# Kernel tuning notes

Hardware: AMD Instinct MI355X
Metric: run time of the kernel (lower is better)

## Reference

```python
import jax, jax.numpy as jnp
import numpy as np

N = 40000      # nodes
E = 320000     # edges (no self loops in input; layer adds them)
F_IN = 256
H1, C1 = 4, 128   # layer 1: att_type 'gat', concat=True
H2, C2 = 8, 6     # layer 2: att_type 'linear', concat=False (mean over heads)
BN_EPS = 1e-5
NEG_SLOPE = 0.2


def setup_inputs() -> dict:
    key = jax.random.key(0)
    k = jax.random.split(key, 12)
    x = jax.random.normal(k[0], (N, F_IN), dtype=jnp.float32)
    row = jax.random.randint(k[1], (E,), 0, N)
    off = jax.random.randint(k[2], (E,), 1, N)
    col = (row + off) % N  # guarantees no self-loops (remove_self_loops is then a no-op)
    edge_index = jnp.stack([row, col])
    s1 = 1.0 / np.sqrt(F_IN)
    s2 = 1.0 / np.sqrt(H1 * C1)
    return dict(
        x=x,
        edge_index=edge_index,
        bn1_gamma=jnp.ones((F_IN,), jnp.float32),
        bn1_beta=jnp.zeros((F_IN,), jnp.float32),
        bn1_mean=jax.random.normal(k[3], (F_IN,), jnp.float32) * 0.1,
        bn1_var=jax.random.uniform(k[4], (F_IN,), jnp.float32, 0.5, 1.5),
        W1=jax.random.normal(k[5], (F_IN, H1 * C1), jnp.float32) * s1,
        att1=jax.random.normal(k[6], (1, H1, 2 * C1), jnp.float32) * 0.1,
        b1=jnp.zeros((H1 * C1,), jnp.float32),
        bn2_gamma=jnp.ones((H1 * C1,), jnp.float32),
        bn2_beta=jnp.zeros((H1 * C1,), jnp.float32),
        bn2_mean=jax.random.normal(k[7], (H1 * C1,), jnp.float32) * 0.1,
        bn2_var=jax.random.uniform(k[8], (H1 * C1,), jnp.float32, 0.5, 1.5),
        W2=jax.random.normal(k[9], (H1 * C1, H2 * C2), jnp.float32) * s2,
        att2=jax.random.normal(k[10], (1, H2, 2 * C2), jnp.float32) * 0.1,
        b2=jnp.zeros((C2,), jnp.float32),
    )


def _bn_eval(x, gamma, beta, mean, var):
    # BatchNorm1d in eval mode (running statistics)
    return (x - mean) * (gamma / jnp.sqrt(var + BN_EPS)) + beta


def _segment_softmax(alpha, seg, num_segments):
    # stable softmax over edges grouped by destination node
    m = jax.ops.segment_max(alpha, seg, num_segments=num_segments)
    ex = jnp.exp(alpha - m[seg])
    den = jax.ops.segment_sum(ex, seg, num_segments=num_segments)
    return ex / (den[seg] + 1e-16)


def _geo_layer(x, row, col, W, att, bias, heads, out_c, att_type, concat):
    n = x.shape[0]
    h = (x @ W).reshape(n, heads, out_c)  # [N,H,C]
    h_j = h[col]                          # gather source features per edge [E,H,C]
    if att_type == 'gat':
        # (cat([x_i,x_j]) * att).sum(-1) == per-node left/right projections gathered
        a_i = (h * att[:, :, :out_c]).sum(-1)[row]   # [E,H]
        a_j = (h_j * att[:, :, out_c:]).sum(-1)      # [E,H]
        alpha = jax.nn.leaky_relu(a_i + a_j, NEG_SLOPE)
    elif att_type == 'linear':
        al = (h_j * att[:, :, :out_c]).sum(-1)
        ar = (h_j * att[:, :, out_c:]).sum(-1)
        alpha = jnp.tanh(al + ar)
    else:
        raise ValueError(att_type)
    alpha = _segment_softmax(alpha, row, n)          # neighbor softmax
    msg = h_j * alpha[:, :, None]                    # [E,H,C]
    out = jax.ops.segment_sum(msg, row, num_segments=n)  # scatter-add ('sum' agg)
    if concat:
        out = out.reshape(n, heads * out_c)
    else:
        out = out.mean(axis=1)
    return out + bias


def reference(x, edge_index, bn1_gamma, bn1_beta, bn1_mean, bn1_var, W1, att1, b1,
              bn2_gamma, bn2_beta, bn2_mean, bn2_var, W2, att2, b2):
    n = x.shape[0]
    loop = jnp.arange(n, dtype=edge_index.dtype)
    row = jnp.concatenate([edge_index[0], loop])  # add self loops (input has none)
    col = jnp.concatenate([edge_index[1], loop])
    # layer 1: dropout (identity in eval) -> BN -> GeoLayer(gat) -> act 'linear' (identity)
    out = _bn_eval(x, bn1_gamma, bn1_beta, bn1_mean, bn1_var)
    out = _geo_layer(out, row, col, W1, att1, b1, H1, C1, 'gat', True)
    # layer 2: BN -> GeoLayer(linear) -> elu
    out = _bn_eval(out, bn2_gamma, bn2_beta, bn2_mean, bn2_var)
    out = jax.nn.elu(_geo_layer(out, row, col, W2, att2, b2, H2, C2, 'linear', False))
    return jax.nn.log_softmax(out, axis=1)
```

## Files before the change

### kernel.cpp

```cpp
#include <hip/hip_runtime.h>
#include <math.h>

#define NN   40000
#define NP   40064
#define EE   320000
#define ET   (EE + NN)
#define FIN  256
#define D1   512
#define NEG  0.2f
#define CAP  64

typedef unsigned short ushort;
typedef __attribute__((ext_vector_type(8))) short   s16x8;
typedef __attribute__((ext_vector_type(4))) float   f32x4;
typedef __attribute__((ext_vector_type(4))) unsigned short u16x4;

#define GL16(g,s) __builtin_amdgcn_global_load_lds((const __attribute__((address_space(1))) unsigned*)(g), (__attribute__((address_space(3))) unsigned*)(s), 16, 0, 0)

__device__ __forceinline__ float lrelu(float x){ return x > 0.f ? x : NEG*x; }
__device__ __forceinline__ float b2f(ushort u){ return __uint_as_float(((unsigned)u) << 16); }
__device__ __forceinline__ ushort f2bf(float f){
  unsigned u = __float_as_uint(f);
  return (ushort)((u + 0x7fffu + ((u >> 16) & 1u)) >> 16);
}
__device__ __forceinline__ float wmaxf(float v){
#pragma unroll
  for (int o = 32; o > 0; o >>= 1) v = fmaxf(v, __shfl_xor(v, o));
  return v;
}
__device__ __forceinline__ float wsumf(float v){
#pragma unroll
  for (int o = 32; o > 0; o >>= 1) v += __shfl_xor(v, o);
  return v;
}

__global__ __launch_bounds__(1024) void zero_prep_kernel(int* __restrict__ cnt,
                            const float* __restrict__ g1, const float* __restrict__ be1,
                            const float* __restrict__ mu1, const float* __restrict__ va1,
                            const float* __restrict__ g2, const float* __restrict__ be2,
                            const float* __restrict__ mu2, const float* __restrict__ va2,
                            const float* __restrict__ b1,
                            float* __restrict__ sc1, float* __restrict__ sh1,
                            float* __restrict__ sc2, float* __restrict__ sh2)
{
  int i = blockIdx.x*1024 + threadIdx.x;
  if (i < NN) cnt[i] = 0;
  if (blockIdx.x == 0){
    int t = threadIdx.x;
    if (t < FIN){ float s = g1[t]*rsqrtf(va1[t]+1e-5f); sc1[t]=s; sh1[t]=be1[t]-mu1[t]*s; }
    if (t < D1){ float s = g2[t]*rsqrtf(va2[t]+1e-5f); sc2[t]=s; sh2[t]=be2[t]+(b1[t]-mu2[t])*s; }
  }
}

__global__ __launch_bounds__(256) void prep_all_kernel(
    const int* __restrict__ rows, const int* __restrict__ cols,
    int* __restrict__ cnt, int* __restrict__ cs,
    const float* __restrict__ W1, const float* __restrict__ W2,
    const float* __restrict__ sc1, const float* __restrict__ sh1,
    const float* __restrict__ sc2, const float* __restrict__ sh2,
    const float* __restrict__ att1, const float* __restrict__ att2,
    ushort* __restrict__ K1T, float* __restrict__ k0v,
    float* __restrict__ c2, float* __restrict__ a2s)
{
  int b = blockIdx.x;
  if (b < 1407){
    int e = b*256 + threadIdx.x;
    if (e >= ET) return;
    int r, c;
    if (e < EE){ r = rows[e]; c = cols[e]; } else { r = e - EE; c = r; }
    int slot = atomicAdd(&cnt[r], 1);
    if (slot < CAP) cs[(r << 6) + slot] = c;
    return;
  }
  if (b < 1631){
    __shared__ float wcol[128];
    __shared__ float red[4];
    int t = b - 1407;
    int k = threadIdx.x;
    float val = 0.f;
    if (t < 200){
      int h;
      if (t < 192){
        h = t & 3; int j = t >> 2;
        if (k < 128){ int kk = h*128 + k; wcol[k] = W2[(size_t)kk*48 + j] * sc2[kk]; }
      } else {
        h = (t - 192) & 3; int off = ((t - 192) >= 4) ? 128 : 0;
        if (k < 128) wcol[k] = att1[h*256 + off + k];
      }
      __syncthreads();
      const float* wr = W1 + (size_t)k*D1 + h*128;
#pragma unroll
      for (int kk = 0; kk < 128; kk += 4){
        float4 wv = *(const float4*)(wr + kk);
        float4 cv = *(const float4*)(wcol + kk);
        val += wv.x*cv.x + wv.y*cv.y + wv.z*cv.z + wv.w*cv.w;
      }
      K1T[(size_t)t*FIN + k] = f2bf(val * sc1[k]);
      float part = wsumf(sh1[k] * val);
      if ((k & 63) == 0) red[k >> 6] = part;
      __syncthreads();
      if (k == 0) k0v[t] = red[0] + red[1] + red[2] + red[3];
    } else {
      K1T[(size_t)t*FIN + k] = 0;
      if (k == 0) k0v[t] = 0.f;
    }
    return;
  }
  {
    int bb = b - 1631;
    if (bb == 0 && threadIdx.x < 48){
      int h = threadIdx.x/6, c = threadIdx.x%6;
      a2s[threadIdx.x] = att2[h*12 + c] + att2[h*12 + 6 + c];
    }
    int w = bb*4 + (threadIdx.x >> 6);
    int lane = threadIdx.x & 63;
    if (w >= 48) return;
    float acc = 0.f;
    for (int k = lane; k < D1; k += 64) acc += sh2[k] * W2[(size_t)k*48 + w];
    acc = wsumf(acc);
    if (lane == 0) c2[w] = acc;
  }
}

__global__ __launch_bounds__(256) void gemmG_mfma(const float* __restrict__ X,
                                                  const ushort* __restrict__ K1T,
                                                  const float* __restrict__ k0v,
                                                  ushort* __restrict__ G,
                                                  float* __restrict__ ai,
                                                  float* __restrict__ aj)
{
  __shared__ ushort As[128*64];
  __shared__ ushort Bs[224*64];
  int row0 = blockIdx.x * 128;
  int tid = threadIdx.x, lane = tid & 63, wave = tid >> 6;
  f32x4 acc[2][13] = {};
  int srow = lane >> 3;
  int scolb = (lane & 7) * 16;
#pragma unroll
  for (int kt = 0; kt < 4; ++kt){
    int k0 = kt*64;
#pragma unroll
    for (int j = 0; j < 4; ++j){
      int c = wave*4 + j;
      int rl = c*8 + srow;
      int rowg = row0 + rl; if (rowg >= NN) rowg = 0;
      int j0 = ((lane & 7) ^ (rl & 7)) * 8;
      const float* src = X + (size_t)rowg*FIN + k0 + j0;
      float4 v0 = *(const float4*)src;
      float4 v1 = *(const float4*)(src + 4);
      s16x8 o;
      o[0]=(short)f2bf(v0.x); o[1]=(short)f2bf(v0.y); o[2]=(short)f2bf(v0.z); o[3]=(short)f2bf(v0.w);
      o[4]=(short)f2bf(v1.x); o[5]=(short)f2bf(v1.y); o[6]=(short)f2bf(v1.z); o[7]=(short)f2bf(v1.w);
      *(s16x8*)((char*)As + c*1024 + lane*16) = o;
    }
#pragma unroll
    for (int j = 0; j < 7; ++j){
      int c = wave*7 + j;
      int row = c*8 + srow;
      int cb = scolb ^ ((row & 7) << 4);
      GL16((const char*)(K1T + (size_t)row*FIN + k0) + cb, (char*)Bs + c*1024);
    }
    __syncthreads();
#pragma unroll
    for (int kk = 0; kk < 2; ++kk){
      int kb = kk*64 + (lane >> 4)*16;
      s16x8 a[2];
#pragma unroll
      for (int mi = 0; mi < 2; ++mi){
        int row = wave*32 + mi*16 + (lane & 15);
        a[mi] = *(const s16x8*)((const char*)As + row*128 + (kb ^ ((row & 7) << 4)));
      }
#pragma unroll
      for (int ni = 0; ni < 13; ++ni){
        int row = ni*16 + (lane & 15);
        s16x8 bfrag = *(const s16x8*)((const char*)Bs + row*128 + (kb ^ ((row & 7) << 4)));
#pragma unroll
        for (int mi = 0; mi < 2; ++mi)
          acc[mi][ni] = __builtin_amdgcn_mfma_f32_16x16x32_bf16(a[mi], bfrag, acc[mi][ni], 0, 0, 0);
      }
    }
    __syncthreads();
  }
  int cl = lane & 15;
#pragma unroll
  for (int mi = 0; mi < 2; ++mi){
#pragma unroll
    for (int ni = 0; ni < 12; ++ni){
      int t = ni*16 + cl;
      float kc = k0v[t];
#pragma unroll
      for (int rr = 0; rr < 4; ++rr){
        int row = row0 + wave*32 + mi*16 + (lane >> 4)*4 + rr;
        G[(size_t)row*192 + t] = f2bf(acc[mi][ni][rr] + kc);
      }
    }
    if (cl < 8){
      float kc = k0v[192 + cl];
#pragma unroll
      for (int rr = 0; rr < 4; ++rr){
        int row = row0 + wave*32 + mi*16 + (lane >> 4)*4 + rr;
        float v = acc[mi][12][rr] + kc;
        if (cl < 4) ai[(size_t)row*4 + cl] = v;
        else        aj[(size_t)row*4 + (cl-4)] = v;
      }
    }
  }
}

__global__ __launch_bounds__(256) void aggA_kernel(const ushort* __restrict__ G,
                                                   const float* __restrict__ ai,
                                                   const float* __restrict__ aj,
                                                   const int* __restrict__ cnt,
                                                   const int* __restrict__ cs,
                                                   const float* __restrict__ c2,
                                                   const float* __restrict__ a2s,
                                                   ushort* __restrict__ PE)
{
  __shared__ float wsh[4][64][4];
  __shared__ int   csh[4][64];
  int lane = threadIdx.x & 63;
  int wave = threadIdx.x >> 6;
  int n = blockIdx.x*4 + wave;
  int deg = cnt[n]; deg = deg > CAP ? CAP : deg;
  float4 an = *(const float4*)(ai + (size_t)n*4);
  bool aclane = lane < 48;
  int lidx = aclane ? lane : 0;
  const char* Gb = (const char*)G + (size_t)lidx*8;
  float acc = 0.f;

  bool act = lane < deg;
  int c = 0;
  float sx=-1e30f, sy=-1e30f, sz=-1e30f, sw=-1e30f;
  if (act){
    c = cs[(n << 6) + lane];
    float4 av = *(const float4*)(aj + (size_t)c*4);
    sx = lrelu(an.x+av.x); sy = lrelu(an.y+av.y);
    sz = lrelu(an.z+av.z); sw = lrelu(an.w+av.w);
  }
  float m0 = wmaxf(sx), m1 = wmaxf(sy), m2 = wmaxf(sz), m3 = wmaxf(sw);
  float e0 = act ? __expf(sx-m0) : 0.f;
  float e1 = act ? __expf(sy-m1) : 0.f;
  float e2 = act ? __expf(sz-m2) : 0.f;
  float e3 = act ? __expf(sw-m3) : 0.f;
  float d0 = wsumf(e0)+1e-16f, d1 = wsumf(e1)+1e-16f;
  float d2 = wsumf(e2)+1e-16f, d3 = wsumf(e3)+1e-16f;
  if (act){
    wsh[wave][lane][0] = e0/d0; wsh[wave][lane][1] = e1/d1;
    wsh[wave][lane][2] = e2/d2; wsh[wave][lane][3] = e3/d3;
    csh[wave][lane] = c*384;
  }
  int e = 0;
  for (; e + 4 <= deg; e += 4){
    int o0 = csh[wave][e],   o1_ = csh[wave][e+1];
    int o2 = csh[wave][e+2], o3  = csh[wave][e+3];
    float4 w0 = *(const float4*)wsh[wave][e];
    float4 w1 = *(const float4*)wsh[wave][e+1];
    float4 w2 = *(const float4*)wsh[wave][e+2];
    float4 w3 = *(const float4*)wsh[wave][e+3];
    u16x4 v0 = *(const u16x4*)(Gb + o0);
    u16x4 v1 = *(const u16x4*)(Gb + o1_);
    u16x4 v2 = *(const u16x4*)(Gb + o2);
    u16x4 v3 = *(const u16x4*)(Gb + o3);
    acc += w0.x*b2f(v0[0]) + w0.y*b2f(v0[1]) + w0.z*b2f(v0[2]) + w0.w*b2f(v0[3]);
    acc += w1.x*b2f(v1[0]) + w1.y*b2f(v1[1]) + w1.z*b2f(v1[2]) + w1.w*b2f(v1[3]);
    acc += w2.x*b2f(v2[0]) + w2.y*b2f(v2[1]) + w2.z*b2f(v2[2]) + w2.w*b2f(v2[3]);
    acc += w3.x*b2f(v3[0]) + w3.y*b2f(v3[1]) + w3.z*b2f(v3[2]) + w3.w*b2f(v3[3]);
  }
  for (; e < deg; ++e){
    int o0 = csh[wave][e];
    float4 w0 = *(const float4*)wsh[wave][e];
    u16x4 v0 = *(const u16x4*)(Gb + o0);
    acc += w0.x*b2f(v0[0]) + w0.y*b2f(v0[1]) + w0.z*b2f(v0[2]) + w0.w*b2f(v0[3]);
  }

  float h = acc + (aclane ? c2[lidx] : 0.f);
  float s = h * (aclane ? a2s[lidx] : 0.f);
  float tot = 0.f;
  int base = (lane/6)*6;
#pragma unroll
  for (int i = 0; i < 6; ++i) tot += __shfl(s, base + i);
  if (aclane){
    float eh = __expf(tanhf(tot));
    ushort* pe = PE + ((size_t)n << 6);
    pe[lane] = f2bf(eh * h);
    if ((lane % 6) == 0) pe[48 + lane/6] = f2bf(eh);
  }
}

__global__ __launch_bounds__(256) void agg2_kernel(const ushort* __restrict__ PE,
                                                   const int* __restrict__ cnt,
                                                   const int* __restrict__ cs,
                                                   const float* __restrict__ bias2,
                                                   float* __restrict__ out)
{
  __shared__ int csh[4][64];
  int lane = threadIdx.x & 63;
  int wave = threadIdx.x >> 6;
  int n = blockIdx.x*4 + wave;
  int deg = cnt[n]; deg = deg > CAP ? CAP : deg;
  int lidx = (lane < 56) ? lane : 0;
  const char* PEb = (const char*)PE + (size_t)lidx*2;
  float acc = 0.f;

  if (lane < deg) csh[wave][lane] = cs[(n << 6) + lane] << 7;
  int e = 0;
  for (; e + 4 <= deg; e += 4){
    int o0 = csh[wave][e],   o1_ = csh[wave][e+1];
    int o2 = csh[wave][e+2], o3  = csh[wave][e+3];
    float v0 = b2f(*(const ushort*)(PEb + o0));
    float v1 = b2f(*(const ushort*)(PEb + o1_));
    float v2 = b2f(*(const ushort*)(PEb + o2));
    float v3 = b2f(*(const ushort*)(PEb + o3));
    acc += (v0 + v1) + (v2 + v3);
  }
  for (; e < deg; ++e)
    acc += b2f(*(const ushort*)(PEb + csh[wave][e]));

  int hh = (lane < 48) ? lane/6 : 0;
  float den = __shfl(acc, 48 + hh);
  float v = acc / den;
  int cc = lane % 6;
  float s = 0.f;
#pragma unroll
  for (int qq = 0; qq < 8; ++qq) s += __shfl(v, cc + 6*qq);
  float val0 = s*(1.f/8.f) + bias2[cc];
  val0 = val0 > 0.f ? val0 : (__expf(val0) - 1.f);
  float val = (lane < 6) ? val0 : -1e30f;
  float mx = val;
#pragma unroll
  for (int o = 1; o < 8; o <<= 1) mx = fmaxf(mx, __shfl_xor(mx, o));
  float ex = (lane < 6) ? __expf(val - mx) : 0.f;
#pragma unroll
  for (int o = 1; o < 8; o <<= 1) ex += __shfl_xor(ex, o);
  if (lane < 6) out[(size_t)n*6 + lane] = val - mx - __logf(ex);
}

extern "C" void kernel_launch(void* const* d_in, const int* in_sizes, int n_in,
                              void* d_out, int out_size, void* d_ws, size_t ws_size,
                              hipStream_t stream)
{
  (void)in_sizes; (void)n_in; (void)out_size; (void)ws_size;
  const float* x   = (const float*)d_in[0];
  const int*   ei  = (const int*)  d_in[1];
  const float* g1  = (const float*)d_in[2];
  const float* be1 = (const float*)d_in[3];
  const float* mu1 = (const float*)d_in[4];
  const float* va1 = (const float*)d_in[5];
  const float* W1  = (const float*)d_in[6];
  const float* at1 = (const float*)d_in[7];
  const float* b1  = (const float*)d_in[8];
  const float* g2  = (const float*)d_in[9];
  const float* be2 = (const float*)d_in[10];
  const float* mu2 = (const float*)d_in[11];
  const float* va2 = (const float*)d_in[12];
  const float* W2  = (const float*)d_in[13];
  const float* at2 = (const float*)d_in[14];
  const float* b2  = (const float*)d_in[15];
  const int* rows = ei;
  const int* cols = ei + EE;
  float* out = (float*)d_out;

  char* p = (char*)d_ws;
  auto carve = [&](size_t bytes)->void*{ void* r = (void*)p; p += (bytes + 255) & ~(size_t)255; return r; };
  ushort* K1T = (ushort*)carve((size_t)224*FIN*2);
  ushort* G   = (ushort*)carve((size_t)NP*192*2);
  ushort* PE  = (ushort*)carve((size_t)NN*64*2);
  float* k0v  = (float*)carve(224*4);
  float* c2   = (float*)carve(48*4);
  float* a2s  = (float*)carve(48*4);
  float* ai   = (float*)carve((size_t)NP*4*4);
  float* aj   = (float*)carve((size_t)NP*4*4);
  float* sc1  = (float*)carve(FIN*4);
  float* sh1  = (float*)carve(FIN*4);
  float* sc2  = (float*)carve(D1*4);
  float* sh2  = (float*)carve(D1*4);
  int* cnt    = (int*)carve((size_t)NN*4);
  int* cs     = (int*)carve((size_t)NN*CAP*4);

  zero_prep_kernel<<<40, 1024, 0, stream>>>(cnt, g1,be1,mu1,va1,g2,be2,mu2,va2,b1,
                                            sc1,sh1,sc2,sh2);
  prep_all_kernel<<<1643, 256, 0, stream>>>(rows, cols, cnt, cs,
                                            W1, W2, sc1, sh1, sc2, sh2, at1, at2,
                                            K1T, k0v, c2, a2s);
  gemmG_mfma<<<313, 256, 0, stream>>>(x, K1T, k0v, G, ai, aj);
  aggA_kernel<<<NN/4, 256, 0, stream>>>(G, ai, aj, cnt, cs, c2, a2s, PE);
  agg2_kernel<<<NN/4, 256, 0, stream>>>(PE, cnt, cs, b2, out);
}
```

Baseline: 103.2 us.

## Halve GEMM row tile to double blocks and unroll gathers by eight

The GEMM kernel's row tile per block goes from 128 to 64 rows, so each wave computes one 16-row MFMA strip and the grid doubles to 626 blocks. On a device with many CUs, 313 blocks underfill the machine. In exchange, the B tile (K1T) is reloaded twice as often and there is less A-fragment reuse per B load. Both aggregation kernels also get an 8-way unrolled gather loop that issues eight independent loads before accumulating, to raise memory-level parallelism on the irregular neighbour reads.

```diff
diff --git a/kernel.cpp b/kernel.cpp
--- a/kernel.cpp
+++ b/kernel.cpp
@@ -129,19 +129,19 @@
                                                   float* __restrict__ ai,
                                                   float* __restrict__ aj)
 {
-  __shared__ ushort As[128*64];
+  __shared__ ushort As[64*64];
   __shared__ ushort Bs[224*64];
-  int row0 = blockIdx.x * 128;
+  int row0 = blockIdx.x * 64;
   int tid = threadIdx.x, lane = tid & 63, wave = tid >> 6;
-  f32x4 acc[2][13] = {};
+  f32x4 acc[13] = {};
   int srow = lane >> 3;
   int scolb = (lane & 7) * 16;
 #pragma unroll
   for (int kt = 0; kt < 4; ++kt){
     int k0 = kt*64;
 #pragma unroll
-    for (int j = 0; j < 4; ++j){
-      int c = wave*4 + j;
+    for (int j = 0; j < 2; ++j){
+      int c = wave*2 + j;
       int rl = c*8 + srow;
       int rowg = row0 + rl; if (rowg >= NN) rowg = 0;
       int j0 = ((lane & 7) ^ (rl & 7)) * 8;
@@ -164,45 +164,36 @@
 #pragma unroll
     for (int kk = 0; kk < 2; ++kk){
       int kb = kk*64 + (lane >> 4)*16;
-      s16x8 a[2];
-#pragma unroll
-      for (int mi = 0; mi < 2; ++mi){
-        int row = wave*32 + mi*16 + (lane & 15);
-        a[mi] = *(const s16x8*)((const char*)As + row*128 + (kb ^ ((row & 7) << 4)));
-      }
+      int arow = wave*16 + (lane & 15);
+      s16x8 a = *(const s16x8*)((const char*)As + arow*128 + (kb ^ ((arow & 7) << 4)));
 #pragma unroll
       for (int ni = 0; ni < 13; ++ni){
         int row = ni*16 + (lane & 15);
         s16x8 bfrag = *(const s16x8*)((const char*)Bs + row*128 + (kb ^ ((row & 7) << 4)));
-#pragma unroll
-        for (int mi = 0; mi < 2; ++mi)
-          acc[mi][ni] = __builtin_amdgcn_mfma_f32_16x16x32_bf16(a[mi], bfrag, acc[mi][ni], 0, 0, 0);
+        acc[ni] = __builtin_amdgcn_mfma_f32_16x16x32_bf16(a, bfrag, acc[ni], 0, 0, 0);
       }
     }
     __syncthreads();
   }
   int cl = lane & 15;
 #pragma unroll
-  for (int mi = 0; mi < 2; ++mi){
-#pragma unroll
-    for (int ni = 0; ni < 12; ++ni){
-      int t = ni*16 + cl;
-      float kc = k0v[t];
-#pragma unroll
-      for (int rr = 0; rr < 4; ++rr){
-        int row = row0 + wave*32 + mi*16 + (lane >> 4)*4 + rr;
-        G[(size_t)row*192 + t] = f2bf(acc[mi][ni][rr] + kc);
-      }
-    }
-    if (cl < 8){
-      float kc = k0v[192 + cl];
-#pragma unroll
-      for (int rr = 0; rr < 4; ++rr){
-        int row = row0 + wave*32 + mi*16 + (lane >> 4)*4 + rr;
-        float v = acc[mi][12][rr] + kc;
-        if (cl < 4) ai[(size_t)row*4 + cl] = v;
-        else        aj[(size_t)row*4 + (cl-4)] = v;
-      }
+  for (int ni = 0; ni < 12; ++ni){
+    int t = ni*16 + cl;
+    float kc = k0v[t];
+#pragma unroll
+    for (int rr = 0; rr < 4; ++rr){
+      int row = row0 + wave*16 + (lane >> 4)*4 + rr;
+      G[(size_t)row*192 + t] = f2bf(acc[ni][rr] + kc);
+    }
+  }
+  if (cl < 8){
+    float kc = k0v[192 + cl];
+#pragma unroll
+    for (int rr = 0; rr < 4; ++rr){
+      int row = row0 + wave*16 + (lane >> 4)*4 + rr;
+      float v = acc[12][rr] + kc;
+      if (cl < 4) ai[(size_t)row*4 + cl] = v;
+      else        aj[(size_t)row*4 + (cl-4)] = v;
     }
   }
 }
@@ -250,6 +241,20 @@
     csh[wave][lane] = c*384;
   }
   int e = 0;
+  for (; e + 8 <= deg; e += 8){
+    int   ob[8];
+    u16x4 vb[8];
+#pragma unroll
+    for (int q = 0; q < 8; ++q) ob[q] = csh[wave][e+q];
+#pragma unroll
+    for (int q = 0; q < 8; ++q) vb[q] = *(const u16x4*)(Gb + ob[q]);
+#pragma unroll
+    for (int q = 0; q < 8; ++q){
+      float4 w = *(const float4*)wsh[wave][e+q];
+      u16x4 v = vb[q];
+      acc += w.x*b2f(v[0]) + w.y*b2f(v[1]) + w.z*b2f(v[2]) + w.w*b2f(v[3]);
+    }
+  }
   for (; e + 4 <= deg; e += 4){
     int o0 = csh[wave][e],   o1_ = csh[wave][e+1];
     int o2 = csh[wave][e+2], o3  = csh[wave][e+3];
@@ -304,6 +309,15 @@
 
   if (lane < deg) csh[wave][lane] = cs[(n << 6) + lane] << 7;
   int e = 0;
+  for (; e + 8 <= deg; e += 8){
+    int ob[8]; ushort vb[8];
+#pragma unroll
+    for (int q = 0; q < 8; ++q) ob[q] = csh[wave][e+q];
+#pragma unroll
+    for (int q = 0; q < 8; ++q) vb[q] = *(const ushort*)(PEb + ob[q]);
+#pragma unroll
+    for (int q = 0; q < 8; ++q) acc += b2f(vb[q]);
+  }
   for (; e + 4 <= deg; e += 4){
     int o0 = csh[wave][e],   o1_ = csh[wave][e+1];
     int o2 = csh[wave][e+2], o3  = csh[wave][e+3];
@@ -382,7 +396,7 @@
   prep_all_kernel<<<1643, 256, 0, stream>>>(rows, cols, cnt, cs,
                                             W1, W2, sc1, sh1, sc2, sh2, at1, at2,
                                             K1T, k0v, c2, a2s);
-  gemmG_mfma<<<313, 256, 0, stream>>>(x, K1T, k0v, G, ai, aj);
+  gemmG_mfma<<<626, 256, 0, stream>>>(x, K1T, k0v, G, ai, aj);
   aggA_kernel<<<NN/4, 256, 0, stream>>>(G, ai, aj, cnt, cs, c2, a2s, PE);
   agg2_kernel<<<NN/4, 256, 0, stream>>>(PE, cnt, cs, b2, out);
 }
```

Measured after the change: 101.6 us. About the same (-1.6%).
